# Kernel optimization log

Hardware: AMD Instinct MI355X
Metric: run time of the kernel (lower is better)

## Reference

```python
import jax, jax.numpy as jnp
import numpy as np

# dims
B, L, D, H, HD, V, FF, NL = 1, 1024, 1024, 16, 64, 32000, 2816, 2
THETA = 500000.0
EPS = 1e-5
BOI, EOI = 31998, 31999
NEG = jnp.float32(-1e30)  # stands in for -inf in the additive mask


def setup_inputs() -> dict:
    key = jax.random.key(0)
    ks = jax.random.split(key, 12)
    tokens = jax.random.randint(ks[0], (B, L), 0, 31998)
    # inject two well-formed image spans per sequence (boi .. eoi)
    tokens = tokens.at[:, 100].set(BOI).at[:, 300].set(EOI)
    tokens = tokens.at[:, 500].set(BOI).at[:, 800].set(EOI)
    s = 0.02
    n = lambda k, shape: (jax.random.normal(k, shape, jnp.float32) * s)
    return {
        "tokens": tokens,
        "tok_emb": n(ks[1], (V, D)),
        "wq": n(ks[2], (NL, D, D)),
        "wk": n(ks[3], (NL, D, D)),
        "wv": n(ks[4], (NL, D, D)),
        "wo": n(ks[5], (NL, D, D)),
        "w1": n(ks[6], (NL, FF, D)),
        "w2": n(ks[7], (NL, D, FF)),
        "w3": n(ks[8], (NL, FF, D)),
        "attn_norm_w": jnp.ones((NL, D), jnp.float32),
        "ffn_norm_w": jnp.ones((NL, D), jnp.float32),
        "final_norm_w": jnp.ones((D,), jnp.float32),
        "w_out": n(ks[9], (V, D)),
    }


def rmsnorm(x, w):
    xf = x.astype(jnp.float32)
    y = xf * jax.lax.rsqrt(jnp.mean(xf * xf, axis=-1, keepdims=True) + EPS)
    return y.astype(x.dtype) * w


def rope_cos_sin():
    inv = 1.0 / (THETA ** (jnp.arange(0, HD, 2, dtype=jnp.float32) / HD))  # [HD/2]
    ang = jnp.arange(L, dtype=jnp.float32)[:, None] * inv[None, :]        # [L, HD/2]
    return jnp.cos(ang), jnp.sin(ang)


def apply_rope(x, cos, sin):
    # x: [B, L, H, HD]; pairs (even, odd) rotated by complex freqs_cis
    xr = x.astype(jnp.float32).reshape(B, L, H, HD // 2, 2)
    xe, xo = xr[..., 0], xr[..., 1]
    c = cos[None, :, None, :]
    s = sin[None, :, None, :]
    out = jnp.stack([xe * c - xo * s, xe * s + xo * c], axis=-1).reshape(B, L, H, HD)
    return out.astype(x.dtype)


def transfusion_mask(tokens):
    # causal everywhere + fully bidirectional within each boi..eoi span
    is_boi = tokens == BOI
    is_eoi = tokens == EOI
    boi_cnt = jnp.cumsum(is_boi.astype(jnp.int32), axis=1)          # inclusive
    eoi_before = jnp.cumsum(is_eoi.astype(jnp.int32), axis=1) - is_eoi.astype(jnp.int32)
    in_span = boi_cnt > eoi_before                                   # [B, L]
    same_span = (in_span[:, :, None] & in_span[:, None, :]) & (
        boi_cnt[:, :, None] == boi_cnt[:, None, :]
    )
    causal = jnp.arange(L)[:, None] >= jnp.arange(L)[None, :]        # [L, L]
    allowed = causal[None] | same_span                                # [B, L, L]
    return jnp.where(allowed, jnp.float32(0.0), NEG)


def reference(tokens, tok_emb, wq, wk, wv, wo, w1, w2, w3,
              attn_norm_w, ffn_norm_w, final_norm_w, w_out):
    h = tok_emb[tokens]                                # [B, L, D]
    cos, sin = rope_cos_sin()
    mask = transfusion_mask(tokens)[:, None]           # [B, 1, L, L]
    scale = 1.0 / jnp.sqrt(jnp.float32(HD))
    for l in range(NL):
        xn = rmsnorm(h, attn_norm_w[l])
        q = (xn @ wq[l].T).reshape(B, L, H, HD)
        k = (xn @ wk[l].T).reshape(B, L, H, HD)
        v = (xn @ wv[l].T).reshape(B, L, H, HD)
        q = apply_rope(q, cos, sin)
        k = apply_rope(k, cos, sin)
        q, k, v = (t.transpose(0, 2, 1, 3) for t in (q, k, v))  # [B, H, L, HD]
        scores = jnp.einsum("bhqd,bhkd->bhqk", q, k) * scale + mask
        p = jax.nn.softmax(scores.astype(jnp.float32), axis=-1).astype(q.dtype)
        attn = jnp.einsum("bhqk,bhkd->bhqd", p, v)
        attn = attn.transpose(0, 2, 1, 3).reshape(B, L, D)
        h = h + attn @ wo[l].T
        xn = rmsnorm(h, ffn_norm_w[l])
        h = h + (jax.nn.silu(xn @ w1[l].T) * (xn @ w3[l].T)) @ w2[l].T
    logits = rmsnorm(h, final_norm_w) @ w_out.T        # [B, L, V]
    return logits
```

## Files before the change

kernel.cpp:

```cpp
#include <hip/hip_runtime.h>
#include <hip/hip_bf16.h>
#include <stdint.h>

typedef unsigned short u16;
typedef __bf16 bf16x8 __attribute__((ext_vector_type(8)));
typedef u16 u16x8 __attribute__((ext_vector_type(8)));
typedef float f32x4 __attribute__((ext_vector_type(4)));

#define SEQ   1024
#define DM    1024
#define NHEADS 16
#define HDIM  64
#define VOC   32000
#define FFD   2816
#define NLAY  2

__device__ __forceinline__ u16 f2b(float f) {
    unsigned x = __builtin_bit_cast(unsigned, f);
    unsigned r = x + 0x7fffu + ((x >> 16) & 1u);
    return (u16)(r >> 16);
}
__device__ __forceinline__ float b2f(u16 u) {
    unsigned x = ((unsigned)u) << 16;
    return __builtin_bit_cast(float, x);
}
__device__ __forceinline__ float grpmax16(float v) {
    v = fmaxf(v, __shfl_xor(v, 1)); v = fmaxf(v, __shfl_xor(v, 2));
    v = fmaxf(v, __shfl_xor(v, 4)); v = fmaxf(v, __shfl_xor(v, 8));
    return v;
}
__device__ __forceinline__ float grpsum16(float v) {
    v += __shfl_xor(v, 1); v += __shfl_xor(v, 2);
    v += __shfl_xor(v, 4); v += __shfl_xor(v, 8);
    return v;
}

__device__ __forceinline__ void gll16(const void* g, void* l) {
    __builtin_amdgcn_global_load_lds(
        (__attribute__((address_space(1))) void*)(uintptr_t)g,
        (__attribute__((address_space(3))) void*)(uint32_t)(uintptr_t)l,
        16, 0, 0);
}
template <int N> __device__ __forceinline__ void vwait() {
    if constexpr (N == 0)       asm volatile("s_waitcnt vmcnt(0)" ::: "memory");
    else if constexpr (N == 4)  asm volatile("s_waitcnt vmcnt(4)" ::: "memory");
    else if constexpr (N == 8)  asm volatile("s_waitcnt vmcnt(8)" ::: "memory");
    else if constexpr (N == 10) asm volatile("s_waitcnt vmcnt(10)" ::: "memory");
    else if constexpr (N == 16) asm volatile("s_waitcnt vmcnt(16)" ::: "memory");
}
__device__ __forceinline__ int xcd_swz(int bid, int nwg) {
    const int q = nwg >> 3, r = nwg & 7;
    const int xcd = bid & 7, j = bid >> 3;
    const int start = (xcd < r) ? xcd * (q + 1) : r * (q + 1) + (xcd - r) * q;
    return start + j;
}

__global__ __launch_bounds__(256) void cvt_kernel(const float* __restrict__ s,
                                                  u16* __restrict__ d, int n8) {
    const int stride = gridDim.x * 256;
    for (int i = blockIdx.x * 256 + threadIdx.x; i < n8; i += stride) {
        const float4 a = ((const float4*)s)[2 * i];
        const float4 b = ((const float4*)s)[2 * i + 1];
        ushort4 p, q;
        p.x = f2b(a.x); p.y = f2b(a.y); p.z = f2b(a.z); p.w = f2b(a.w);
        q.x = f2b(b.x); q.y = f2b(b.y); q.z = f2b(b.z); q.w = f2b(b.w);
        ((ushort4*)d)[2 * i] = p;
        ((ushort4*)d)[2 * i + 1] = q;
    }
}

__global__ __launch_bounds__(256) void embed_kernel(const int* __restrict__ tok,
    const float* __restrict__ emb, float* __restrict__ h) {
    const int l = blockIdx.x;
    const int t = tok[l];
    ((float4*)(h + (size_t)l * DM))[threadIdx.x] =
        ((const float4*)(emb + (size_t)t * DM))[threadIdx.x];
}

__global__ __launch_bounds__(256) void ropetab_kernel(float* __restrict__ cosb,
                                                      float* __restrict__ sinb) {
    const int idx = blockIdx.x * 256 + threadIdx.x;
    const int l = idx >> 5, j = idx & 31;
    const float inv = __expf(-((float)j * (1.0f / 32.0f)) * 13.122363377404328f);
    const float ang = (float)l * inv;
    cosb[idx] = cosf(ang);
    sinb[idx] = sinf(ang);
}

__global__ void span_kernel(const int* __restrict__ tok, int* __restrict__ span) {
    __shared__ int sb[SEQ], se[SEQ];
    const int t = threadIdx.x;
    const int v = tok[t];
    const int bo = (v == 31998) ? 1 : 0;
    const int eo = (v == 31999) ? 1 : 0;
    sb[t] = bo; se[t] = eo;
    __syncthreads();
    for (int o = 1; o < SEQ; o <<= 1) {
        int a = 0, b = 0;
        if (t >= o) { a = sb[t - o]; b = se[t - o]; }
        __syncthreads();
        sb[t] += a; se[t] += b;
        __syncthreads();
    }
    const int bc = sb[t];
    const int ec = se[t] - eo;
    span[t] = (bc > ec) ? bc : 0;
}

__global__ __launch_bounds__(256) void rmsnorm_kernel(const float* __restrict__ x,
    const float* __restrict__ w, u16* __restrict__ o) {
    const int row = blockIdx.x;
    const float4 xv = ((const float4*)(x + (size_t)row * DM))[threadIdx.x];
    float ss = xv.x * xv.x + xv.y * xv.y + xv.z * xv.z + xv.w * xv.w;
    for (int off = 32; off; off >>= 1) ss += __shfl_xor(ss, off);
    __shared__ float red[4];
    const int lane = threadIdx.x & 63, wvi = threadIdx.x >> 6;
    if (lane == 0) red[wvi] = ss;
    __syncthreads();
    const float tot = red[0] + red[1] + red[2] + red[3];
    const float sc = rsqrtf(tot * (1.0f / (float)DM) + 1e-5f);
    const float4 wv4 = ((const float4*)w)[threadIdx.x];
    ushort4 ov;
    ov.x = f2b(xv.x * sc * wv4.x);
    ov.y = f2b(xv.y * sc * wv4.y);
    ov.z = f2b(xv.z * sc * wv4.z);
    ov.w = f2b(xv.w * sc * wv4.w);
    ((ushort4*)(o + (size_t)row * DM))[threadIdx.x] = ov;
}


template <int RESID, int BM, int BN>
__global__ __launch_bounds__(256) void gemm_p_kernel(const u16* __restrict__ A,
    const u16* __restrict__ B, float* __restrict__ C, const float* __restrict__ res,
    int N, int K) {
    constexpr int AL = BM / 32, BL = BN / 32, LOADS = AL + BL;
    constexpr int MF = BM / 32, NF = BN / 32;
    __shared__ __align__(16) u16 sA[2][BM * 64];
    __shared__ __align__(16) u16 sB[2][BN * 64];
    const int nwg = gridDim.x * gridDim.y;
    const int lid = xcd_swz(blockIdx.y * gridDim.x + blockIdx.x, nwg);
    const int tm = (lid % gridDim.x) * BM, tn = (lid / gridDim.x) * BN;
    const int tid = threadIdx.x, lane = tid & 63, wid = tid >> 6;
    const int wm = wid >> 1, wn = wid & 1, fr = lane & 15, g = lane >> 4;

    const u16* ap[AL]; const u16* bp[BL];
#pragma unroll
    for (int j = 0; j < AL; ++j) {
        const int idx = j * 256 + tid, r = idx >> 3, gr = (idx & 7) ^ (r & 7);
        ap[j] = A + (size_t)(tm + r) * K + gr * 8;
    }
#pragma unroll
    for (int j = 0; j < BL; ++j) {
        const int idx = j * 256 + tid, r = idx >> 3, gr = (idx & 7) ^ (r & 7);
        bp[j] = B + (size_t)(tn + r) * K + gr * 8;
    }

    f32x4 acc[MF][NF] = {};
    const int NT = K >> 6;
#pragma unroll
    for (int j = 0; j < AL; ++j) gll16(ap[j], &sA[0][(j * 256 + tid) * 8]);
#pragma unroll
    for (int j = 0; j < BL; ++j) gll16(bp[j], &sB[0][(j * 256 + tid) * 8]);

    int p = 0;
    for (int t = 0; t < NT; ++t) {
        if (t + 1 < NT) {
#pragma unroll
            for (int j = 0; j < AL; ++j) gll16(ap[j] + (t + 1) * 64, &sA[p ^ 1][(j * 256 + tid) * 8]);
#pragma unroll
            for (int j = 0; j < BL; ++j) gll16(bp[j] + (t + 1) * 64, &sB[p ^ 1][(j * 256 + tid) * 8]);
            vwait<LOADS>();
        } else {
            vwait<0>();
        }
        __builtin_amdgcn_s_barrier();
        __builtin_amdgcn_sched_barrier(0);
        bf16x8 af[MF][2], bfv[NF][2];
#pragma unroll
        for (int m = 0; m < MF; ++m)
#pragma unroll
            for (int ks = 0; ks < 2; ++ks) {
                const int row = wm * (BM / 2) + m * 16 + fr;
                const int gr = (ks * 4 + g) ^ (row & 7);
                af[m][ks] = *(const bf16x8*)&sA[p][row * 64 + gr * 8];
            }
#pragma unroll
        for (int n = 0; n < NF; ++n)
#pragma unroll
            for (int ks = 0; ks < 2; ++ks) {
                const int row = wn * (BN / 2) + n * 16 + fr;
                const int gr = (ks * 4 + g) ^ (row & 7);
                bfv[n][ks] = *(const bf16x8*)&sB[p][row * 64 + gr * 8];
            }
        __builtin_amdgcn_s_setprio(1);
#pragma unroll
        for (int m = 0; m < MF; ++m)
#pragma unroll
            for (int n = 0; n < NF; ++n)
#pragma unroll
                for (int ks = 0; ks < 2; ++ks)
                    acc[m][n] = __builtin_amdgcn_mfma_f32_16x16x32_bf16(af[m][ks], bfv[n][ks], acc[m][n], 0, 0, 0);
        __builtin_amdgcn_s_setprio(0);
        __builtin_amdgcn_s_barrier();
        p ^= 1;
    }

    const int cr = (lane >> 4) * 4, cc = lane & 15;
#pragma unroll
    for (int m = 0; m < MF; ++m)
#pragma unroll
        for (int n = 0; n < NF; ++n) {
            const int row0 = tm + wm * (BM / 2) + m * 16 + cr;
            const int col = tn + wn * (BN / 2) + n * 16 + cc;
#pragma unroll
            for (int r = 0; r < 4; ++r) {
                const size_t idx = (size_t)(row0 + r) * N + col;
                float v = acc[m][n][r];
                if (RESID) v += res[idx];
                C[idx] = v;
            }
        }
}

template <int RESID>
__global__ __launch_bounds__(512, 2) void gemm_big_kernel(const u16* __restrict__ A,
    const u16* __restrict__ B, float* __restrict__ C, const float* __restrict__ res,
    int N, int K) {
    __shared__ __align__(16) u16 sA[2][256 * 64];
    __shared__ __align__(16) u16 sB[2][256 * 64];
    const int nwg = gridDim.x * gridDim.y;
    const int lid = xcd_swz(blockIdx.y * gridDim.x + blockIdx.x, nwg);
    const int tm = (lid % gridDim.x) * 256;
    const int tn = (lid / gridDim.x) * 256;
    const int tid = threadIdx.x, lane = tid & 63, wid = tid >> 6;
    const int wm = wid >> 2, wn = wid & 3;
    const int fr = lane & 15, g = lane >> 4;

    const u16* ap[4]; const u16* bp[4];
#pragma unroll
    for (int j = 0; j < 4; ++j) {
        const int idx = j * 512 + tid, r = idx >> 3, gr = (idx & 7) ^ (r & 7);
        ap[j] = A + (size_t)(tm + r) * K + gr * 8;
        bp[j] = B + (size_t)(tn + r) * K + gr * 8;
    }

    f32x4 acc[8][4] = {};
    const int NT = K >> 6;
#pragma unroll
    for (int j = 0; j < 4; ++j) gll16(ap[j], &sA[0][(j * 512 + tid) * 8]);
#pragma unroll
    for (int j = 0; j < 4; ++j) gll16(bp[j], &sB[0][(j * 512 + tid) * 8]);

    int p = 0;
    for (int t = 0; t < NT; ++t) {
        if (t + 1 < NT) {
#pragma unroll
            for (int j = 0; j < 4; ++j) gll16(ap[j] + (t + 1) * 64, &sA[p ^ 1][(j * 512 + tid) * 8]);
#pragma unroll
            for (int j = 0; j < 4; ++j) gll16(bp[j] + (t + 1) * 64, &sB[p ^ 1][(j * 512 + tid) * 8]);
            vwait<8>();
        } else {
            vwait<0>();
        }
        __builtin_amdgcn_s_barrier();
        __builtin_amdgcn_sched_barrier(0);
        bf16x8 bfv[4][2];
#pragma unroll
        for (int n = 0; n < 4; ++n)
#pragma unroll
            for (int ks = 0; ks < 2; ++ks) {
                const int row = wn * 64 + n * 16 + fr;
                const int gr = (ks * 4 + g) ^ (row & 7);
                bfv[n][ks] = *(const bf16x8*)&sB[p][row * 64 + gr * 8];
            }
#pragma unroll
        for (int mq = 0; mq < 4; ++mq) {
            bf16x8 af[2][2];
#pragma unroll
            for (int i = 0; i < 2; ++i)
#pragma unroll
                for (int ks = 0; ks < 2; ++ks) {
                    const int row = wm * 128 + (mq * 2 + i) * 16 + fr;
                    const int gr = (ks * 4 + g) ^ (row & 7);
                    af[i][ks] = *(const bf16x8*)&sA[p][row * 64 + gr * 8];
                }
            __builtin_amdgcn_s_setprio(1);
#pragma unroll
            for (int i = 0; i < 2; ++i)
#pragma unroll
                for (int n = 0; n < 4; ++n)
#pragma unroll
                    for (int ks = 0; ks < 2; ++ks)
                        acc[mq * 2 + i][n] = __builtin_amdgcn_mfma_f32_16x16x32_bf16(
                            af[i][ks], bfv[n][ks], acc[mq * 2 + i][n], 0, 0, 0);
            __builtin_amdgcn_s_setprio(0);
        }
        __builtin_amdgcn_s_barrier();
        p ^= 1;
    }

    const int cr = (lane >> 4) * 4, cc = lane & 15;
#pragma unroll
    for (int m = 0; m < 8; ++m)
#pragma unroll
        for (int n = 0; n < 4; ++n) {
            const int row0 = tm + wm * 128 + m * 16 + cr;
            const int col = tn + wn * 64 + n * 16 + cc;
#pragma unroll
            for (int r = 0; r < 4; ++r) {
                const size_t idx = (size_t)(row0 + r) * N + col;
                float v = acc[m][n][r];
                if (RESID) v += res[idx];
                C[idx] = v;
            }
        }
}

__global__ __launch_bounds__(256) void qkv_kernel(const u16* __restrict__ A,
    const u16* __restrict__ Bq, const u16* __restrict__ Bk, const u16* __restrict__ Bv,
    const float* __restrict__ cosb, const float* __restrict__ sinb,
    u16* __restrict__ qb, u16* __restrict__ kb, u16* __restrict__ vb) {
    __shared__ __align__(16) u16 sA[2][128 * 64];
    __shared__ __align__(16) u16 sB[2][128 * 64];
    const int lid = xcd_swz(blockIdx.y * gridDim.x + blockIdx.x, 8 * 24);
    const int tm = (lid % 8) * 128;
    const int yy = lid / 8;
    const int mat = yy >> 3;
    const int tn = (yy & 7) * 128;
    const u16* B = (mat == 0) ? Bq : (mat == 1) ? Bk : Bv;
    u16* out = (mat == 0) ? qb : (mat == 1) ? kb : vb;
    const int tid = threadIdx.x, lane = tid & 63, wid = tid >> 6;
    const int wm = wid >> 1, wn = wid & 1, fr = lane & 15, g = lane >> 4;

    const u16* ap[4]; const u16* bp[4];
#pragma unroll
    for (int j = 0; j < 4; ++j) {
        const int idx = j * 256 + tid, r = idx >> 3, gr = (idx & 7) ^ (r & 7);
        ap[j] = A + (size_t)(tm + r) * DM + gr * 8;
        bp[j] = B + (size_t)(tn + r) * DM + gr * 8;
    }

    f32x4 acc[4][4] = {};
#pragma unroll
    for (int j = 0; j < 4; ++j) gll16(ap[j], &sA[0][(j * 256 + tid) * 8]);
#pragma unroll
    for (int j = 0; j < 4; ++j) gll16(bp[j], &sB[0][(j * 256 + tid) * 8]);

    int p = 0;
    for (int t = 0; t < DM / 64; ++t) {
        if (t + 1 < DM / 64) {
#pragma unroll
            for (int j = 0; j < 4; ++j) gll16(ap[j] + (t + 1) * 64, &sA[p ^ 1][(j * 256 + tid) * 8]);
#pragma unroll
            for (int j = 0; j < 4; ++j) gll16(bp[j] + (t + 1) * 64, &sB[p ^ 1][(j * 256 + tid) * 8]);
            vwait<8>();
        } else {
            vwait<0>();
        }
        __builtin_amdgcn_s_barrier();
        __builtin_amdgcn_sched_barrier(0);
        bf16x8 af[4][2], bfv[4][2];
#pragma unroll
        for (int m = 0; m < 4; ++m)
#pragma unroll
            for (int ks = 0; ks < 2; ++ks) {
                const int row = wm * 64 + m * 16 + fr;
                const int gr = (ks * 4 + g) ^ (row & 7);
                af[m][ks] = *(const bf16x8*)&sA[p][row * 64 + gr * 8];
            }
#pragma unroll
        for (int n = 0; n < 4; ++n)
#pragma unroll
            for (int ks = 0; ks < 2; ++ks) {
                const int row = wn * 64 + n * 16 + fr;
                const int gr = (ks * 4 + g) ^ (row & 7);
                bfv[n][ks] = *(const bf16x8*)&sB[p][row * 64 + gr * 8];
            }
        __builtin_amdgcn_s_setprio(1);
#pragma unroll
        for (int m = 0; m < 4; ++m)
#pragma unroll
            for (int n = 0; n < 4; ++n)
#pragma unroll
                for (int ks = 0; ks < 2; ++ks)
                    acc[m][n] = __builtin_amdgcn_mfma_f32_16x16x32_bf16(af[m][ks], bfv[n][ks], acc[m][n], 0, 0, 0);
        __builtin_amdgcn_s_setprio(0);
        __builtin_amdgcn_s_barrier();
        p ^= 1;
    }

    const int cr = (lane >> 4) * 4, cc = lane & 15;
    if (mat < 2) {
#pragma unroll
        for (int m = 0; m < 4; ++m)
#pragma unroll
            for (int n = 0; n < 4; ++n) {
                const int row0 = tm + wm * 64 + m * 16 + cr;
                const int col = tn + wn * 64 + n * 16 + cc;
                const int j = (n * 16 + cc) >> 1;
#pragma unroll
                for (int r = 0; r < 4; ++r) {
                    const int row = row0 + r;
                    const float c = cosb[row * 32 + j];
                    const float s = sinb[row * 32 + j];
                    const float v = acc[m][n][r];
                    const float pv = __shfl_xor(v, 1);
                    const float o = (cc & 1) ? (pv * s + v * c) : (v * c - pv * s);
                    out[(size_t)row * DM + col] = f2b(o);
                }
            }
    } else {
#pragma unroll
        for (int m = 0; m < 4; ++m)
#pragma unroll
            for (int n = 0; n < 4; ++n) {
                const int row0 = tm + wm * 64 + m * 16 + cr;
                const int col = tn + wn * 64 + n * 16 + cc;
#pragma unroll
                for (int r = 0; r < 4; ++r)
                    out[(size_t)(row0 + r) * DM + col] = f2b(acc[m][n][r]);
            }
    }
}

__global__ __launch_bounds__(256) void ffn13_kernel(const u16* __restrict__ A,
    const u16* __restrict__ B1, const u16* __restrict__ B3, u16* __restrict__ Z) {
    __shared__ __align__(16) u16 sA[2][64 * 64];
    __shared__ __align__(16) u16 sB1[2][128 * 64];
    __shared__ __align__(16) u16 sB3[2][128 * 64];
    const int lid = xcd_swz(blockIdx.y * gridDim.x + blockIdx.x, 16 * 22);
    const int tm = (lid % 16) * 64;
    const int tn = (lid / 16) * 128;
    const int tid = threadIdx.x, lane = tid & 63, wid = tid >> 6;
    const int wm = wid >> 1, wn = wid & 1, fr = lane & 15, g = lane >> 4;

    const u16* ap[2]; const u16* b1p[4]; const u16* b3p[4];
#pragma unroll
    for (int j = 0; j < 2; ++j) {
        const int idx = j * 256 + tid, r = idx >> 3, gr = (idx & 7) ^ (r & 7);
        ap[j] = A + (size_t)(tm + r) * DM + gr * 8;
    }
#pragma unroll
    for (int j = 0; j < 4; ++j) {
        const int idx = j * 256 + tid, r = idx >> 3, gr = (idx & 7) ^ (r & 7);
        b1p[j] = B1 + (size_t)(tn + r) * DM + gr * 8;
        b3p[j] = B3 + (size_t)(tn + r) * DM + gr * 8;
    }

    f32x4 acc1[2][4] = {}, acc3[2][4] = {};
#pragma unroll
    for (int j = 0; j < 2; ++j) gll16(ap[j], &sA[0][(j * 256 + tid) * 8]);
#pragma unroll
    for (int j = 0; j < 4; ++j) gll16(b1p[j], &sB1[0][(j * 256 + tid) * 8]);
#pragma unroll
    for (int j = 0; j < 4; ++j) gll16(b3p[j], &sB3[0][(j * 256 + tid) * 8]);

    int p = 0;
    for (int t = 0; t < DM / 64; ++t) {
        if (t + 1 < DM / 64) {
#pragma unroll
            for (int j = 0; j < 2; ++j) gll16(ap[j] + (t + 1) * 64, &sA[p ^ 1][(j * 256 + tid) * 8]);
#pragma unroll
            for (int j = 0; j < 4; ++j) gll16(b1p[j] + (t + 1) * 64, &sB1[p ^ 1][(j * 256 + tid) * 8]);
#pragma unroll
            for (int j = 0; j < 4; ++j) gll16(b3p[j] + (t + 1) * 64, &sB3[p ^ 1][(j * 256 + tid) * 8]);
            vwait<10>();
        } else {
            vwait<0>();
        }
        __builtin_amdgcn_s_barrier();
        __builtin_amdgcn_sched_barrier(0);
        bf16x8 af[2][2], b1v[4][2], b3v[4][2];
#pragma unroll
        for (int m = 0; m < 2; ++m)
#pragma unroll
            for (int ks = 0; ks < 2; ++ks) {
                const int row = wm * 32 + m * 16 + fr;
                const int gr = (ks * 4 + g) ^ (row & 7);
                af[m][ks] = *(const bf16x8*)&sA[p][row * 64 + gr * 8];
            }
#pragma unroll
        for (int n = 0; n < 4; ++n)
#pragma unroll
            for (int ks = 0; ks < 2; ++ks) {
                const int row = wn * 64 + n * 16 + fr;
                const int gr = (ks * 4 + g) ^ (row & 7);
                b1v[n][ks] = *(const bf16x8*)&sB1[p][row * 64 + gr * 8];
                b3v[n][ks] = *(const bf16x8*)&sB3[p][row * 64 + gr * 8];
            }
        __builtin_amdgcn_s_setprio(1);
#pragma unroll
        for (int m = 0; m < 2; ++m)
#pragma unroll
            for (int n = 0; n < 4; ++n)
#pragma unroll
                for (int ks = 0; ks < 2; ++ks) {
                    acc1[m][n] = __builtin_amdgcn_mfma_f32_16x16x32_bf16(af[m][ks], b1v[n][ks], acc1[m][n], 0, 0, 0);
                    acc3[m][n] = __builtin_amdgcn_mfma_f32_16x16x32_bf16(af[m][ks], b3v[n][ks], acc3[m][n], 0, 0, 0);
                }
        __builtin_amdgcn_s_setprio(0);
        __builtin_amdgcn_s_barrier();
        p ^= 1;
    }

    const int cr = (lane >> 4) * 4, cc = lane & 15;
#pragma unroll
    for (int m = 0; m < 2; ++m)
#pragma unroll
        for (int n = 0; n < 4; ++n) {
            const int row0 = tm + wm * 32 + m * 16 + cr;
            const int col = tn + wn * 64 + n * 16 + cc;
#pragma unroll
            for (int r = 0; r < 4; ++r) {
                const float a1 = acc1[m][n][r];
                const float a3 = acc3[m][n][r];
                const float z = a1 / (1.f + __expf(-a1)) * a3;
                Z[(size_t)(row0 + r) * FFD + col] = f2b(z);
            }
        }
}

__global__ __launch_bounds__(256) void fattn_kernel(const u16* __restrict__ qb,
    const u16* __restrict__ kb, const u16* __restrict__ vb,
    const int* __restrict__ span, u16* __restrict__ ob) {
    __shared__ __align__(16) u16 sK[64][72];
    __shared__ __align__(16) u16 sVT[64][72];
    __shared__ __align__(16) u16 sP[4][16][72];
    const int tid = threadIdx.x, lane = tid & 63, wq = tid >> 6;
    const int g = lane >> 4, fr = lane & 15;
    const int head = blockIdx.y;
    const int qbase = blockIdx.x * 64;

    bf16x8 qfr[2];
    {
        const u16* qp = qb + (size_t)(qbase + wq * 16 + fr) * DM + head * HDIM + g * 8;
        qfr[0] = *(const bf16x8*)(qp);
        qfr[1] = *(const bf16x8*)(qp + 32);
    }
    int sq[4];
#pragma unroll
    for (int r = 0; r < 4; ++r) sq[r] = span[qbase + wq * 16 + g * 4 + r];

    float m_old[4] = {-1e30f, -1e30f, -1e30f, -1e30f};
    float lsum[4] = {0.f, 0.f, 0.f, 0.f};
    f32x4 acc[4] = {};

    for (int kb0 = 0; kb0 < SEQ; kb0 += 64) {
        __syncthreads();
        {
            const int r = tid >> 2, c0 = (tid & 3) * 16;
            const u16* src = kb + (size_t)(kb0 + r) * DM + head * HDIM + c0;
            *(u16x8*)&sK[r][c0]     = *(const u16x8*)(src);
            *(u16x8*)&sK[r][c0 + 8] = *(const u16x8*)(src + 8);
        }
        {
            const int k = tid & 63, d0 = (tid >> 6) * 16;
            const u16* src = vb + (size_t)(kb0 + k) * DM + head * HDIM + d0;
            const u16x8 v0 = *(const u16x8*)(src);
            const u16x8 v1 = *(const u16x8*)(src + 8);
#pragma unroll
            for (int j = 0; j < 8; ++j) {
                sVT[d0 + j][k]     = v0[j];
                sVT[d0 + 8 + j][k] = v1[j];
            }
        }
        __syncthreads();

        f32x4 accs[4] = {};
        __builtin_amdgcn_s_setprio(1);
#pragma unroll
        for (int nf = 0; nf < 4; ++nf)
#pragma unroll
            for (int kf = 0; kf < 2; ++kf) {
                const bf16x8 kfv = *(const bf16x8*)&sK[nf * 16 + fr][g * 8 + kf * 32];
                accs[nf] = __builtin_amdgcn_mfma_f32_16x16x32_bf16(qfr[kf], kfv, accs[nf], 0, 0, 0);
            }
        __builtin_amdgcn_s_setprio(0);

        int spk[4];
#pragma unroll
        for (int nf = 0; nf < 4; ++nf) spk[nf] = span[kb0 + nf * 16 + fr];
        float sv[4][4]; bool al[4][4];
#pragma unroll
        for (int nf = 0; nf < 4; ++nf) {
            const int key = kb0 + nf * 16 + fr;
#pragma unroll
            for (int r = 0; r < 4; ++r) {
                const int q = qbase + wq * 16 + g * 4 + r;
                al[nf][r] = (key <= q) || (sq[r] > 0 && spk[nf] == sq[r]);
                sv[nf][r] = al[nf][r] ? accs[nf][r] * 0.125f : -1e30f;
            }
        }
        float alpha[4], ls[4];
#pragma unroll
        for (int r = 0; r < 4; ++r) {
            float mn = fmaxf(fmaxf(sv[0][r], sv[1][r]), fmaxf(sv[2][r], sv[3][r]));
            mn = grpmax16(mn);
            const float mnew = fmaxf(m_old[r], mn);
            alpha[r] = __expf(m_old[r] - mnew);
            m_old[r] = mnew;
            ls[r] = 0.f;
        }
        u16 pb[4][4];
#pragma unroll
        for (int nf = 0; nf < 4; ++nf)
#pragma unroll
            for (int r = 0; r < 4; ++r) {
                const float p = al[nf][r] ? __expf(sv[nf][r] - m_old[r]) : 0.f;
                ls[r] += p;
                pb[nf][r] = f2b(p);
            }
#pragma unroll
        for (int r = 0; r < 4; ++r) {
            lsum[r] = lsum[r] * alpha[r] + grpsum16(ls[r]);
#pragma unroll
            for (int nf = 0; nf < 4; ++nf) acc[nf][r] *= alpha[r];
        }
#pragma unroll
        for (int nf = 0; nf < 4; ++nf)
#pragma unroll
            for (int r = 0; r < 4; ++r)
                sP[wq][g * 4 + r][nf * 16 + fr] = pb[nf][r];

        __builtin_amdgcn_s_setprio(1);
#pragma unroll
        for (int nf = 0; nf < 4; ++nf)
#pragma unroll
            for (int kf = 0; kf < 2; ++kf) {
                const bf16x8 pa  = *(const bf16x8*)&sP[wq][fr][g * 8 + kf * 32];
                const bf16x8 vtb = *(const bf16x8*)&sVT[nf * 16 + fr][g * 8 + kf * 32];
                acc[nf] = __builtin_amdgcn_mfma_f32_16x16x32_bf16(pa, vtb, acc[nf], 0, 0, 0);
            }
        __builtin_amdgcn_s_setprio(0);
    }

#pragma unroll
    for (int nf = 0; nf < 4; ++nf)
#pragma unroll
        for (int r = 0; r < 4; ++r) {
            const int q = qbase + wq * 16 + g * 4 + r;
            const int d = nf * 16 + fr;
            ob[(size_t)q * DM + head * HDIM + d] = f2b(acc[nf][r] / lsum[r]);
        }
}

extern "C" void kernel_launch(void* const* d_in, const int* in_sizes, int n_in,
                              void* d_out, int out_size, void* d_ws, size_t ws_size,
                              hipStream_t stream) {
    (void)in_sizes; (void)n_in; (void)out_size; (void)ws_size;
    const int*   tokens   = (const int*)d_in[0];
    const float* tok_emb  = (const float*)d_in[1];
    const float* wq       = (const float*)d_in[2];
    const float* wk       = (const float*)d_in[3];
    const float* wvw      = (const float*)d_in[4];
    const float* wo       = (const float*)d_in[5];
    const float* w1       = (const float*)d_in[6];
    const float* w2       = (const float*)d_in[7];
    const float* w3       = (const float*)d_in[8];
    const float* attn_nw  = (const float*)d_in[9];
    const float* ffn_nw   = (const float*)d_in[10];
    const float* final_nw = (const float*)d_in[11];
    const float* w_out    = (const float*)d_in[12];
    float* logits = (float*)d_out;

    char* ws = (char*)d_ws;
    size_t off = 0;
    auto alloc = [&](size_t b) { size_t o = off; off += (b + 255) & ~(size_t)255; return o; };
    float* h    = (float*)(ws + alloc((size_t)SEQ * DM * 4));
    u16*   xn   = (u16*)  (ws + alloc((size_t)SEQ * DM * 2));
    u16*   qb   = (u16*)  (ws + alloc((size_t)SEQ * DM * 2));
    u16*   kb   = (u16*)  (ws + alloc((size_t)SEQ * DM * 2));
    u16*   vb   = (u16*)  (ws + alloc((size_t)SEQ * DM * 2));
    u16*   ab   = (u16*)  (ws + alloc((size_t)SEQ * DM * 2));
    u16*   zb   = (u16*)  (ws + alloc((size_t)SEQ * FFD * 2));
    float* cosb = (float*)(ws + alloc((size_t)SEQ * 32 * 4));
    float* sinb = (float*)(ws + alloc((size_t)SEQ * 32 * 4));
    int*   span = (int*)  (ws + alloc((size_t)SEQ * 4));
    const size_t nQ = (size_t)NLAY * DM * DM;
    const size_t nF = (size_t)NLAY * FFD * DM;
    const size_t nO = (size_t)VOC * DM;
    u16* wqb = (u16*)(ws + alloc(nQ * 2));
    u16* wkb = (u16*)(ws + alloc(nQ * 2));
    u16* wvb = (u16*)(ws + alloc(nQ * 2));
    u16* wob = (u16*)(ws + alloc(nQ * 2));
    u16* w1b = (u16*)(ws + alloc(nF * 2));
    u16* w2b = (u16*)(ws + alloc(nF * 2));
    u16* w3b = (u16*)(ws + alloc(nF * 2));
    u16* woub = (u16*)(ws + alloc(nO * 2));

    auto cvt = [&](const float* s, u16* d, size_t n) {
        const int n8 = (int)(n / 8);
        const int blocks = (n8 + 255) / 256 < 2048 ? (n8 + 255) / 256 : 2048;
        cvt_kernel<<<blocks, 256, 0, stream>>>(s, d, n8);
    };
    cvt(wq, wqb, nQ); cvt(wk, wkb, nQ); cvt(wvw, wvb, nQ); cvt(wo, wob, nQ);
    cvt(w1, w1b, nF); cvt(w2, w2b, nF); cvt(w3, w3b, nF);
    cvt(w_out, woub, nO);

    embed_kernel<<<SEQ, 256, 0, stream>>>(tokens, tok_emb, h);
    ropetab_kernel<<<(SEQ * 32) / 256, 256, 0, stream>>>(cosb, sinb);
    span_kernel<<<1, SEQ, 0, stream>>>(tokens, span);

    for (int l = 0; l < NLAY; ++l) {
        rmsnorm_kernel<<<SEQ, 256, 0, stream>>>(h, attn_nw + (size_t)l * DM, xn);
        qkv_kernel<<<dim3(8, 24), 256, 0, stream>>>(
            xn, wqb + (size_t)l * DM * DM, wkb + (size_t)l * DM * DM, wvb + (size_t)l * DM * DM,
            cosb, sinb, qb, kb, vb);
        fattn_kernel<<<dim3(SEQ / 64, NHEADS), 256, 0, stream>>>(qb, kb, vb, span, ab);
        gemm_p_kernel<1, 64, 64><<<dim3(16, 16), 256, 0, stream>>>(
            ab, wob + (size_t)l * DM * DM, h, h, DM, DM);

        rmsnorm_kernel<<<SEQ, 256, 0, stream>>>(h, ffn_nw + (size_t)l * DM, xn);
        ffn13_kernel<<<dim3(16, 22), 256, 0, stream>>>(
            xn, w1b + (size_t)l * FFD * DM, w3b + (size_t)l * FFD * DM, zb);
        gemm_p_kernel<1, 64, 64><<<dim3(16, 16), 256, 0, stream>>>(
            zb, w2b + (size_t)l * DM * FFD, h, h, DM, FFD);
    }

    rmsnorm_kernel<<<SEQ, 256, 0, stream>>>(h, final_nw, xn);
    gemm_big_kernel<0><<<dim3(SEQ / 256, VOC / 256), 512, 0, stream>>>(
        xn, woub, logits, nullptr, VOC, DM);
}
```

Baseline: 426.2 us.

## Skip masked attention key tiles, batch weight conversions, split barriers in vocab GEMM

The span kernel now builds a per-64-token bitmask of which image spans each tile touches. The attention kernel uses it to skip key tiles that lie entirely in the causal future and share no bidirectional span with the query tile. Tiles fully below the diagonal also skip the per-element mask evaluation. The eight separate fp32-to-bf16 weight conversion launches are merged into one launch. The large output GEMM now loads its B fragments inside the first mq iteration and puts a barrier after each mq step, which adds synchronisation inside the inner loop.

```diff
diff --git a/kernel.cpp b/kernel.cpp
--- a/kernel.cpp
+++ b/kernel.cpp
@@ -55,17 +55,22 @@
     return start + j;
 }
 
-__global__ __launch_bounds__(256) void cvt_kernel(const float* __restrict__ s,
-                                                  u16* __restrict__ d, int n8) {
+struct CvtArgs { const float* s[8]; u16* d[8]; int n8[8]; };
+__global__ __launch_bounds__(256) void cvt_all_kernel(CvtArgs a) {
     const int stride = gridDim.x * 256;
-    for (int i = blockIdx.x * 256 + threadIdx.x; i < n8; i += stride) {
-        const float4 a = ((const float4*)s)[2 * i];
-        const float4 b = ((const float4*)s)[2 * i + 1];
-        ushort4 p, q;
-        p.x = f2b(a.x); p.y = f2b(a.y); p.z = f2b(a.z); p.w = f2b(a.w);
-        q.x = f2b(b.x); q.y = f2b(b.y); q.z = f2b(b.z); q.w = f2b(b.w);
-        ((ushort4*)d)[2 * i] = p;
-        ((ushort4*)d)[2 * i + 1] = q;
+    for (int g = 0; g < 8; ++g) {
+        const float* __restrict__ s = a.s[g];
+        u16* __restrict__ d = a.d[g];
+        const int n8 = a.n8[g];
+        for (int i = blockIdx.x * 256 + threadIdx.x; i < n8; i += stride) {
+            const float4 x = ((const float4*)s)[2 * i];
+            const float4 y = ((const float4*)s)[2 * i + 1];
+            ushort4 p, q;
+            p.x = f2b(x.x); p.y = f2b(x.y); p.z = f2b(x.z); p.w = f2b(x.w);
+            q.x = f2b(y.x); q.y = f2b(y.y); q.z = f2b(y.z); q.w = f2b(y.w);
+            ((ushort4*)d)[2 * i] = p;
+            ((ushort4*)d)[2 * i + 1] = q;
+        }
     }
 }
 
@@ -87,13 +92,16 @@
     sinb[idx] = sinf(ang);
 }
 
-__global__ void span_kernel(const int* __restrict__ tok, int* __restrict__ span) {
+__global__ void span_kernel(const int* __restrict__ tok, int* __restrict__ span,
+                            int* __restrict__ tmask) {
     __shared__ int sb[SEQ], se[SEQ];
+    __shared__ int tm[SEQ / 64];
     const int t = threadIdx.x;
     const int v = tok[t];
     const int bo = (v == 31998) ? 1 : 0;
     const int eo = (v == 31999) ? 1 : 0;
     sb[t] = bo; se[t] = eo;
+    if (t < SEQ / 64) tm[t] = 0;
     __syncthreads();
     for (int o = 1; o < SEQ; o <<= 1) {
         int a = 0, b = 0;
@@ -104,7 +112,11 @@
     }
     const int bc = sb[t];
     const int ec = se[t] - eo;
-    span[t] = (bc > ec) ? bc : 0;
+    const int id = (bc > ec) ? bc : 0;
+    span[t] = id;
+    if (id > 0) atomicOr(&tm[t >> 6], 1 << ((id - 1) & 31));
+    __syncthreads();
+    if (t < SEQ / 64) tmask[t] = tm[t];
 }
 
 __global__ __launch_bounds__(256) void rmsnorm_kernel(const float* __restrict__ x,
@@ -266,15 +278,17 @@
         __builtin_amdgcn_sched_barrier(0);
         bf16x8 bfv[4][2];
 #pragma unroll
-        for (int n = 0; n < 4; ++n)
-#pragma unroll
-            for (int ks = 0; ks < 2; ++ks) {
-                const int row = wn * 64 + n * 16 + fr;
-                const int gr = (ks * 4 + g) ^ (row & 7);
-                bfv[n][ks] = *(const bf16x8*)&sB[p][row * 64 + gr * 8];
-            }
-#pragma unroll
         for (int mq = 0; mq < 4; ++mq) {
+            if (mq == 0) {
+#pragma unroll
+                for (int n = 0; n < 4; ++n)
+#pragma unroll
+                    for (int ks = 0; ks < 2; ++ks) {
+                        const int row = wn * 64 + n * 16 + fr;
+                        const int gr = (ks * 4 + g) ^ (row & 7);
+                        bfv[n][ks] = *(const bf16x8*)&sB[p][row * 64 + gr * 8];
+                    }
+            }
             bf16x8 af[2][2];
 #pragma unroll
             for (int i = 0; i < 2; ++i)
@@ -294,8 +308,8 @@
                         acc[mq * 2 + i][n] = __builtin_amdgcn_mfma_f32_16x16x32_bf16(
                             af[i][ks], bfv[n][ks], acc[mq * 2 + i][n], 0, 0, 0);
             __builtin_amdgcn_s_setprio(0);
-        }
-        __builtin_amdgcn_s_barrier();
+            __builtin_amdgcn_s_barrier();
+        }
         p ^= 1;
     }
 
@@ -522,7 +536,7 @@
 
 __global__ __launch_bounds__(256) void fattn_kernel(const u16* __restrict__ qb,
     const u16* __restrict__ kb, const u16* __restrict__ vb,
-    const int* __restrict__ span, u16* __restrict__ ob) {
+    const int* __restrict__ span, const int* __restrict__ tmask, u16* __restrict__ ob) {
     __shared__ __align__(16) u16 sK[64][72];
     __shared__ __align__(16) u16 sVT[64][72];
     __shared__ __align__(16) u16 sP[4][16][72];
@@ -530,6 +544,7 @@
     const int g = lane >> 4, fr = lane & 15;
     const int head = blockIdx.y;
     const int qbase = blockIdx.x * 64;
+    const int qmask = tmask[blockIdx.x];
 
     bf16x8 qfr[2];
     {
@@ -545,7 +560,9 @@
     float lsum[4] = {0.f, 0.f, 0.f, 0.f};
     f32x4 acc[4] = {};
 
-    for (int kb0 = 0; kb0 < SEQ; kb0 += 64) {
+    for (int kt = 0; kt < SEQ / 64; ++kt) {
+        const int kb0 = kt * 64;
+        if (kb0 > qbase && (qmask & tmask[kt]) == 0) continue;
         __syncthreads();
         {
             const int r = tid >> 2, c0 = (tid & 3) * 16;
@@ -577,18 +594,28 @@
             }
         __builtin_amdgcn_s_setprio(0);
 
-        int spk[4];
-#pragma unroll
-        for (int nf = 0; nf < 4; ++nf) spk[nf] = span[kb0 + nf * 16 + fr];
         float sv[4][4]; bool al[4][4];
-#pragma unroll
-        for (int nf = 0; nf < 4; ++nf) {
-            const int key = kb0 + nf * 16 + fr;
-#pragma unroll
-            for (int r = 0; r < 4; ++r) {
-                const int q = qbase + wq * 16 + g * 4 + r;
-                al[nf][r] = (key <= q) || (sq[r] > 0 && spk[nf] == sq[r]);
-                sv[nf][r] = al[nf][r] ? accs[nf][r] * 0.125f : -1e30f;
+        if (kb0 + 63 <= qbase) {
+#pragma unroll
+            for (int nf = 0; nf < 4; ++nf)
+#pragma unroll
+                for (int r = 0; r < 4; ++r) {
+                    al[nf][r] = true;
+                    sv[nf][r] = accs[nf][r] * 0.125f;
+                }
+        } else {
+            int spk[4];
+#pragma unroll
+            for (int nf = 0; nf < 4; ++nf) spk[nf] = span[kb0 + nf * 16 + fr];
+#pragma unroll
+            for (int nf = 0; nf < 4; ++nf) {
+                const int key = kb0 + nf * 16 + fr;
+#pragma unroll
+                for (int r = 0; r < 4; ++r) {
+                    const int q = qbase + wq * 16 + g * 4 + r;
+                    al[nf][r] = (key <= q) || (sq[r] > 0 && spk[nf] == sq[r]);
+                    sv[nf][r] = al[nf][r] ? accs[nf][r] * 0.125f : -1e30f;
+                }
             }
         }
         float alpha[4], ls[4];
@@ -676,6 +703,7 @@
     float* cosb = (float*)(ws + alloc((size_t)SEQ * 32 * 4));
     float* sinb = (float*)(ws + alloc((size_t)SEQ * 32 * 4));
     int*   span = (int*)  (ws + alloc((size_t)SEQ * 4));
+    int*   tmask= (int*)  (ws + alloc((size_t)(SEQ / 64) * 4));
     const size_t nQ = (size_t)NLAY * DM * DM;
     const size_t nF = (size_t)NLAY * FFD * DM;
     const size_t nO = (size_t)VOC * DM;
@@ -688,25 +716,27 @@
     u16* w3b = (u16*)(ws + alloc(nF * 2));
     u16* woub = (u16*)(ws + alloc(nO * 2));
 
-    auto cvt = [&](const float* s, u16* d, size_t n) {
-        const int n8 = (int)(n / 8);
-        const int blocks = (n8 + 255) / 256 < 2048 ? (n8 + 255) / 256 : 2048;
-        cvt_kernel<<<blocks, 256, 0, stream>>>(s, d, n8);
-    };
-    cvt(wq, wqb, nQ); cvt(wk, wkb, nQ); cvt(wvw, wvb, nQ); cvt(wo, wob, nQ);
-    cvt(w1, w1b, nF); cvt(w2, w2b, nF); cvt(w3, w3b, nF);
-    cvt(w_out, woub, nO);
+    CvtArgs ca;
+    ca.s[0] = wq;  ca.d[0] = wqb;  ca.n8[0] = (int)(nQ / 8);
+    ca.s[1] = wk;  ca.d[1] = wkb;  ca.n8[1] = (int)(nQ / 8);
+    ca.s[2] = wvw; ca.d[2] = wvb;  ca.n8[2] = (int)(nQ / 8);
+    ca.s[3] = wo;  ca.d[3] = wob;  ca.n8[3] = (int)(nQ / 8);
+    ca.s[4] = w1;  ca.d[4] = w1b;  ca.n8[4] = (int)(nF / 8);
+    ca.s[5] = w2;  ca.d[5] = w2b;  ca.n8[5] = (int)(nF / 8);
+    ca.s[6] = w3;  ca.d[6] = w3b;  ca.n8[6] = (int)(nF / 8);
+    ca.s[7] = w_out; ca.d[7] = woub; ca.n8[7] = (int)(nO / 8);
+    cvt_all_kernel<<<2048, 256, 0, stream>>>(ca);
 
     embed_kernel<<<SEQ, 256, 0, stream>>>(tokens, tok_emb, h);
     ropetab_kernel<<<(SEQ * 32) / 256, 256, 0, stream>>>(cosb, sinb);
-    span_kernel<<<1, SEQ, 0, stream>>>(tokens, span);
+    span_kernel<<<1, SEQ, 0, stream>>>(tokens, span, tmask);
 
     for (int l = 0; l < NLAY; ++l) {
         rmsnorm_kernel<<<SEQ, 256, 0, stream>>>(h, attn_nw + (size_t)l * DM, xn);
         qkv_kernel<<<dim3(8, 24), 256, 0, stream>>>(
             xn, wqb + (size_t)l * DM * DM, wkb + (size_t)l * DM * DM, wvb + (size_t)l * DM * DM,
             cosb, sinb, qb, kb, vb);
-        fattn_kernel<<<dim3(SEQ / 64, NHEADS), 256, 0, stream>>>(qb, kb, vb, span, ab);
+        fattn_kernel<<<dim3(SEQ / 64, NHEADS), 256, 0, stream>>>(qb, kb, vb, span, tmask, ab);
         gemm_p_kernel<1, 64, 64><<<dim3(16, 16), 256, 0, stream>>>(
             ab, wob + (size_t)l * DM * DM, h, h, DM, DM);
 
```

Result: faster. 384.8 us (-9.7%).
